# Kernel tuning notes

Hardware: AMD Instinct MI355X
Metric: run time of the kernel (lower is better)

The kernel has to match this reference:

```python
import jax, jax.numpy as jnp
import numpy as np

LN_EPS = 1e-5


def _make_valid_boxes(key, shape):
    # boxes in [x_min, y_min, x_max, y_max] with min < max
    k1, k2 = jax.random.split(key)
    mins = jax.random.uniform(k1, shape, dtype=jnp.float32)            # [.., 2]
    sizes = jax.random.uniform(k2, shape, dtype=jnp.float32) * 0.2 + 1e-3
    return jnp.concatenate([mins, mins + sizes], axis=-1)


def setup_inputs() -> dict:
    key = jax.random.key(0)
    k_t, k_b, k_w = jax.random.split(key, 3)
    N, H = 100000, 768
    target = _make_valid_boxes(k_t, (2,))          # [4]
    ocr_boxes = _make_valid_boxes(k_b, (N, 2))     # [N, 4]
    W = jax.random.normal(k_w, (11, H), dtype=jnp.float32) * (1.0 / np.sqrt(11))
    b = jnp.zeros((H,), dtype=jnp.float32)
    ln_gamma = jnp.ones((H,), dtype=jnp.float32)
    ln_beta = jnp.zeros((H,), dtype=jnp.float32)
    return {"target": target, "ocr_boxes": ocr_boxes, "W": W, "b": b,
            "ln_gamma": ln_gamma, "ln_beta": ln_beta}


def _geo_features(target, boxes):
    # target: [4], boxes: [N, 4]  (x_min, y_min, x_max, y_max)
    tx0, ty0, tx1, ty1 = target[0], target[1], target[2], target[3]
    x0, y0, x1, y1 = boxes[:, 0], boxes[:, 1], boxes[:, 2], boxes[:, 3]
    N = boxes.shape[0]
    ones = jnp.ones((N,), boxes.dtype)

    # HeightWidthRelation: [w1, h1, w2, h2, |w1-w2|, |h1-h2|]
    w1, h1 = tx1 - tx0, ty1 - ty0
    w2, h2 = x1 - x0, y1 - y0
    hw = jnp.stack([w1 * ones, h1 * ones, w2, h2,
                    jnp.abs(w1 - w2), jnp.abs(h1 - h2)], axis=-1)   # [N, 6]

    # Centers
    c1x, c1y = (tx0 + tx1) * 0.5, (ty0 + ty1) * 0.5
    c2x, c2y = (x0 + x1) * 0.5, (y0 + y1) * 0.5
    dx, dy = c2x - c1x, c2y - c1y

    # DistanceRelation: L2 center distance
    dist = jnp.sqrt(dx * dx + dy * dy)                               # [N]

    # IoURelation
    overlap = (tx0 < x1) & (tx1 > x0) & (ty0 < y1) & (ty1 > y0)
    xi0, yi0 = jnp.maximum(tx0, x0), jnp.maximum(ty0, y0)
    xi1, yi1 = jnp.minimum(tx1, x1), jnp.minimum(ty1, y1)
    inter = jnp.where(overlap, (xi1 - xi0) * (yi1 - yi0), 0.0)       # [N]
    a1 = w1 * h1
    a2 = w2 * h2
    union = a1 + a2 - inter
    iou = jnp.stack([inter / union, inter / a1, inter / a2], axis=-1)  # [N, 3]

    # AngleRelation: atan2(|dy|, |dx|) degree bucket (degree in [0, 90])
    degree = jnp.arctan2(jnp.abs(dy), jnp.abs(dx)) * (180.0 / jnp.pi)
    bucket = jnp.where((degree > 22.5) & (degree <= 67.5), 1.0,
             jnp.where((degree > 67.5) & (degree <= 112.5), 2.0,
             jnp.where((degree > 112.5) & (degree <= 157.5), 3.0,
             jnp.where((degree > 157.5) & (degree <= 202.5), 4.0,
             jnp.where((degree > 202.5) & (degree <= 247.5), 5.0,
             jnp.where((degree > 247.5) & (degree <= 292.5), 6.0,
             jnp.where((degree > 292.5) & (degree <= 337.5), 7.0, 8.0)))))))

    return jnp.concatenate([hw, dist[:, None], iou, bucket[:, None]], axis=-1)  # [N, 11]


def reference(target, ocr_boxes, W, b, ln_gamma, ln_beta):
    feats = _geo_features(target, ocr_boxes)            # [N, 11]
    x = feats @ W + b                                   # [N, H]
    mean = jnp.mean(x, axis=-1, keepdims=True)
    var = jnp.mean(jnp.square(x - mean), axis=-1, keepdims=True)
    x = (x - mean) * jax.lax.rsqrt(var + LN_EPS) * ln_gamma + ln_beta
    return jax.nn.relu(x)
```

## Files before the change

### kernel.cpp

```cpp
#include <hip/hip_runtime.h>
#include <math.h>

#define H 768
#define LN_EPS 1e-5f

typedef float nfloat4 __attribute__((ext_vector_type(4)));

__global__ __launch_bounds__(256, 2) void geo_ln_kernel(
    const float* __restrict__ target,
    const float* __restrict__ boxes,
    const float* __restrict__ W,
    const float* __restrict__ bias,
    const float* __restrict__ gamma,
    const float* __restrict__ beta,
    float* __restrict__ out,
    int N)
{
    const int lane = threadIdx.x & 63;
    const int wid  = (blockIdx.x << 2) | (threadIdx.x >> 6);
    const int nw   = gridDim.x << 2;

    const float tx0 = target[0], ty0 = target[1], tx1 = target[2], ty1 = target[3];
    const float w1 = tx1 - tx0, h1 = ty1 - ty0;
    const float c1x = (tx0 + tx1) * 0.5f, c1y = (ty0 + ty1) * 0.5f;
    const float a1 = w1 * h1;
    const float ra1 = 1.0f / a1;
    const float tanA = 0.41421356237309503f;
    const float tanB = 2.41421356237309503f;

    const float4* __restrict__ W4  = reinterpret_cast<const float4*>(W);
    const float4* __restrict__ b4  = reinterpret_cast<const float4*>(bias);
    const float4* __restrict__ g4  = reinterpret_cast<const float4*>(gamma);
    const float4* __restrict__ be4 = reinterpret_cast<const float4*>(beta);
    const float4* __restrict__ boxes4 = reinterpret_cast<const float4*>(boxes);
    nfloat4* __restrict__ outv = reinterpret_cast<nfloat4*>(out);

    float4 base[3], Wr[3][9], gm[3], bt[3];
    #pragma unroll
    for (int r = 0; r < 3; ++r) {
        const int c4 = lane + 64 * r;
        float4 acc = b4[c4];
        const float4 w0 = W4[0 * (H / 4) + c4];
        const float4 w1r = W4[1 * (H / 4) + c4];
        acc.x = fmaf(w1, w0.x, acc.x); acc.y = fmaf(w1, w0.y, acc.y);
        acc.z = fmaf(w1, w0.z, acc.z); acc.w = fmaf(w1, w0.w, acc.w);
        acc.x = fmaf(h1, w1r.x, acc.x); acc.y = fmaf(h1, w1r.y, acc.y);
        acc.z = fmaf(h1, w1r.z, acc.z); acc.w = fmaf(h1, w1r.w, acc.w);
        base[r] = acc;
        #pragma unroll
        for (int k = 0; k < 9; ++k)
            Wr[r][k] = W4[(k + 2) * (H / 4) + c4];
        gm[r] = g4[c4];
        bt[r] = be4[c4];
    }

    auto process = [&](int box) {
        const float4 bx = boxes4[box];
        const float x0 = bx.x, y0 = bx.y, x1 = bx.z, y1 = bx.w;

        float v[9];
        const float w2 = x1 - x0, h2 = y1 - y0;
        v[0] = w2; v[1] = h2;
        v[2] = fabsf(w1 - w2); v[3] = fabsf(h1 - h2);
        const float c2x = (x0 + x1) * 0.5f, c2y = (y0 + y1) * 0.5f;
        const float dx = c2x - c1x, dy = c2y - c1y;
        v[4] = __builtin_amdgcn_sqrtf(dx * dx + dy * dy);
        const bool overlap = (tx0 < x1) && (tx1 > x0) && (ty0 < y1) && (ty1 > y0);
        const float xi0 = fmaxf(tx0, x0), yi0 = fmaxf(ty0, y0);
        const float xi1 = fminf(tx1, x1), yi1 = fminf(ty1, y1);
        const float inter = overlap ? (xi1 - xi0) * (yi1 - yi0) : 0.0f;
        const float a2 = w2 * h2;
        const float uni = a1 + a2 - inter;
        v[5] = inter * __builtin_amdgcn_rcpf(uni);
        v[6] = inter * ra1;
        v[7] = inter * __builtin_amdgcn_rcpf(a2);
        const float adx = fabsf(dx), ady = fabsf(dy);
        v[8] = (ady > adx * tanA) ? ((ady > adx * tanB) ? 2.0f : 1.0f) : 8.0f;

        float4 xv[3];
        float s = 0.0f, sq = 0.0f;
        #pragma unroll
        for (int r = 0; r < 3; ++r) {
            float4 acc = base[r];
            #pragma unroll
            for (int k = 0; k < 9; ++k) {
                const float4 w = Wr[r][k];
                acc.x = fmaf(v[k], w.x, acc.x);
                acc.y = fmaf(v[k], w.y, acc.y);
                acc.z = fmaf(v[k], w.z, acc.z);
                acc.w = fmaf(v[k], w.w, acc.w);
            }
            xv[r] = acc;
            s  += acc.x + acc.y + acc.z + acc.w;
            sq += acc.x * acc.x + acc.y * acc.y + acc.z * acc.z + acc.w * acc.w;
        }

        #pragma unroll
        for (int off = 32; off >= 1; off >>= 1) {
            s  += __shfl_xor(s,  off, 64);
            sq += __shfl_xor(sq, off, 64);
        }
        const float mean = s * (1.0f / H);
        const float var  = sq * (1.0f / H) - mean * mean;
        const float rstd = __builtin_amdgcn_rsqf(var + LN_EPS);

        nfloat4* __restrict__ orow = outv + (size_t)box * (H / 4);
        #pragma unroll
        for (int r = 0; r < 3; ++r) {
            const float4 vx = xv[r];
            const float4 g = gm[r], be = bt[r];
            nfloat4 o;
            o.x = fmaxf(0.0f, (vx.x - mean) * rstd * g.x + be.x);
            o.y = fmaxf(0.0f, (vx.y - mean) * rstd * g.y + be.y);
            o.z = fmaxf(0.0f, (vx.z - mean) * rstd * g.z + be.z);
            o.w = fmaxf(0.0f, (vx.w - mean) * rstd * g.w + be.w);
            __builtin_nontemporal_store(o, &orow[lane + 64 * r]);
        }
    };

    int box = wid;
    for (; box + nw < N; box += 2 * nw) {
        process(box);
        process(box + nw);
    }
    if (box < N) process(box);
}

extern "C" void kernel_launch(void* const* d_in, const int* in_sizes, int n_in,
                              void* d_out, int out_size, void* d_ws, size_t ws_size,
                              hipStream_t stream) {
    const float* target = (const float*)d_in[0];
    const float* boxes  = (const float*)d_in[1];
    const float* W      = (const float*)d_in[2];
    const float* bias   = (const float*)d_in[3];
    const float* gamma  = (const float*)d_in[4];
    const float* beta   = (const float*)d_in[5];
    float* out = (float*)d_out;

    const int N = in_sizes[1] / 4;
    const int grid = 512;

    geo_ln_kernel<<<grid, 256, 0, stream>>>(target, boxes, W, bias, gamma, beta, out, N);
}
```

Baseline: 350.4 us.

## Compute LayerNorm stats analytically via Gram matrix of W and bias

Precomputes the Gram matrix of the weight rows and bias, plus their column means, in a small kernel. A second kernel derives each row's mean and variance in closed form from the 11 features, so the main kernel no longer needs the 64-lane shuffle reductions. The main kernel also prefetches the next boxes and stats one iteration ahead. This adds two extra launches and a stats round-trip through workspace memory, and the E[x^2]-mean^2 form may lose precision.

Measured after the change: 324.5 us. 7.4% less time.

```diff
diff --git a/kernel.cpp b/kernel.cpp
--- a/kernel.cpp
+++ b/kernel.cpp
@@ -6,7 +6,230 @@
 
 typedef float nfloat4 __attribute__((ext_vector_type(4)));
 
+__device__ __forceinline__ void geo_feats(
+    const float4 bx,
+    const float tx0, const float ty0, const float tx1, const float ty1,
+    const float w1, const float h1, const float c1x, const float c1y,
+    const float a1, const float ra1,
+    float* __restrict__ v)
+{
+    const float tanA = 0.41421356237309503f;
+    const float tanB = 2.41421356237309503f;
+    const float x0 = bx.x, y0 = bx.y, x1 = bx.z, y1 = bx.w;
+    const float w2 = x1 - x0, h2 = y1 - y0;
+    v[0] = w2; v[1] = h2;
+    v[2] = fabsf(w1 - w2); v[3] = fabsf(h1 - h2);
+    const float c2x = (x0 + x1) * 0.5f, c2y = (y0 + y1) * 0.5f;
+    const float dx = c2x - c1x, dy = c2y - c1y;
+    v[4] = __builtin_amdgcn_sqrtf(dx * dx + dy * dy);
+    const bool overlap = (tx0 < x1) && (tx1 > x0) && (ty0 < y1) && (ty1 > y0);
+    const float xi0 = fmaxf(tx0, x0), yi0 = fmaxf(ty0, y0);
+    const float xi1 = fminf(tx1, x1), yi1 = fminf(ty1, y1);
+    const float inter = overlap ? (xi1 - xi0) * (yi1 - yi0) : 0.0f;
+    const float a2 = w2 * h2;
+    const float uni = a1 + a2 - inter;
+    v[5] = inter * __builtin_amdgcn_rcpf(uni);
+    v[6] = inter * ra1;
+    v[7] = inter * __builtin_amdgcn_rcpf(a2);
+    const float adx = fabsf(dx), ady = fabsf(dy);
+    v[8] = (ady > adx * tanA) ? ((ady > adx * tanB) ? 2.0f : 1.0f) : 8.0f;
+}
+
+__global__ __launch_bounds__(256) void gram_kernel(
+    const float* __restrict__ W,
+    const float* __restrict__ bias,
+    float* __restrict__ ws)
+{
+    const int i = blockIdx.x;
+    const int tid = threadIdx.x;
+
+    int p = 0, q = 0;
+    const float* A;
+    const float* B = nullptr;
+    if (i < 78) {
+        while ((p + 1) * (p + 2) / 2 <= i) ++p;
+        q = i - p * (p + 1) / 2;
+        A = (p < 11) ? (W + p * H) : bias;
+        B = (q < 11) ? (W + q * H) : bias;
+    } else {
+        p = i - 78;
+        A = (p < 11) ? (W + p * H) : bias;
+    }
+
+    float acc = 0.0f;
+    if (B) {
+        for (int c = tid; c < H; c += 256) acc += A[c] * B[c];
+    } else {
+        for (int c = tid; c < H; c += 256) acc += A[c];
+    }
+
+    #pragma unroll
+    for (int off = 32; off >= 1; off >>= 1) acc += __shfl_xor(acc, off, 64);
+
+    __shared__ float red[4];
+    if ((tid & 63) == 0) red[tid >> 6] = acc;
+    __syncthreads();
+    if (tid == 0) {
+        const float s = ((red[0] + red[1]) + (red[2] + red[3])) * (1.0f / H);
+        if (i < 78) { ws[p * 12 + q] = s; ws[q * 12 + p] = s; }
+        else        { ws[144 + p] = s; }
+    }
+}
+
+__global__ __launch_bounds__(256) void stats_kernel(
+    const float* __restrict__ target,
+    const float* __restrict__ boxes,
+    const float* __restrict__ ws,
+    float2* __restrict__ stats,
+    int N)
+{
+    const float tx0 = target[0], ty0 = target[1], tx1 = target[2], ty1 = target[3];
+    const float w1 = tx1 - tx0, h1 = ty1 - ty0;
+    const float c1x = (tx0 + tx1) * 0.5f, c1y = (ty0 + ty1) * 0.5f;
+    const float a1 = w1 * h1;
+    const float ra1 = 1.0f / a1;
+
+    float Q[9][9], qlin[9], mlin[9];
+    #pragma unroll
+    for (int l = 0; l < 9; ++l)
+        #pragma unroll
+        for (int k = 0; k < 9; ++k)
+            Q[l][k] = ws[(l + 2) * 12 + (k + 2)];
+    #pragma unroll
+    for (int k = 0; k < 9; ++k) {
+        qlin[k] = 2.0f * (w1 * ws[0 * 12 + (k + 2)]
+                        + h1 * ws[1 * 12 + (k + 2)]
+                        +      ws[11 * 12 + (k + 2)]);
+        mlin[k] = ws[144 + k + 2];
+    }
+    const float K = w1 * w1 * ws[0] + 2.0f * w1 * h1 * ws[1] + h1 * h1 * ws[13]
+                  + 2.0f * w1 * ws[11] + 2.0f * h1 * ws[1 * 12 + 11] + ws[11 * 12 + 11];
+    const float mconst = w1 * ws[144] + h1 * ws[145] + ws[155];
+
+    const float4* __restrict__ boxes4 = reinterpret_cast<const float4*>(boxes);
+    const int stride = gridDim.x * blockDim.x;
+    for (int b = blockIdx.x * blockDim.x + threadIdx.x; b < N; b += stride) {
+        const float4 bx = boxes4[b];
+        float v[9];
+        geo_feats(bx, tx0, ty0, tx1, ty1, w1, h1, c1x, c1y, a1, ra1, v);
+
+        float mean = mconst;
+        #pragma unroll
+        for (int k = 0; k < 9; ++k) mean = fmaf(mlin[k], v[k], mean);
+
+        float E = K;
+        #pragma unroll
+        for (int l = 0; l < 9; ++l) {
+            float t = qlin[l];
+            #pragma unroll
+            for (int k = 0; k < 9; ++k) t = fmaf(Q[l][k], v[k], t);
+            E = fmaf(t, v[l], E);
+        }
+
+        const float var  = fmaf(-mean, mean, E);
+        const float rstd = __builtin_amdgcn_rsqf(fmaxf(var, 0.0f) + LN_EPS);
+        float2 st; st.x = rstd; st.y = mean * rstd;
+        stats[b] = st;
+    }
+}
+
 __global__ __launch_bounds__(256, 2) void geo_ln_kernel(
+    const float* __restrict__ target,
+    const float* __restrict__ boxes,
+    const float* __restrict__ W,
+    const float* __restrict__ bias,
+    const float* __restrict__ gamma,
+    const float* __restrict__ beta,
+    const float2* __restrict__ stats,
+    float* __restrict__ out,
+    int N)
+{
+    const int lane = threadIdx.x & 63;
+    const int wid  = (blockIdx.x << 2) | (threadIdx.x >> 6);
+    const int nw   = gridDim.x << 2;
+
+    const float tx0 = target[0], ty0 = target[1], tx1 = target[2], ty1 = target[3];
+    const float w1 = tx1 - tx0, h1 = ty1 - ty0;
+    const float c1x = (tx0 + tx1) * 0.5f, c1y = (ty0 + ty1) * 0.5f;
+    const float a1 = w1 * h1;
+    const float ra1 = 1.0f / a1;
+
+    const float4* __restrict__ W4  = reinterpret_cast<const float4*>(W);
+    const float4* __restrict__ b4  = reinterpret_cast<const float4*>(bias);
+    const float4* __restrict__ g4  = reinterpret_cast<const float4*>(gamma);
+    const float4* __restrict__ be4 = reinterpret_cast<const float4*>(beta);
+    const float4* __restrict__ boxes4 = reinterpret_cast<const float4*>(boxes);
+    nfloat4* __restrict__ outv = reinterpret_cast<nfloat4*>(out);
+
+    float4 base[3], Wr[3][9], gm[3], bt[3];
+    #pragma unroll
+    for (int r = 0; r < 3; ++r) {
+        const int c4 = lane + 64 * r;
+        float4 acc = b4[c4];
+        const float4 w0  = W4[0 * (H / 4) + c4];
+        const float4 w1r = W4[1 * (H / 4) + c4];
+        acc.x = fmaf(w1, w0.x, acc.x); acc.y = fmaf(w1, w0.y, acc.y);
+        acc.z = fmaf(w1, w0.z, acc.z); acc.w = fmaf(w1, w0.w, acc.w);
+        acc.x = fmaf(h1, w1r.x, acc.x); acc.y = fmaf(h1, w1r.y, acc.y);
+        acc.z = fmaf(h1, w1r.z, acc.z); acc.w = fmaf(h1, w1r.w, acc.w);
+        base[r] = acc;
+        #pragma unroll
+        for (int k = 0; k < 9; ++k)
+            Wr[r][k] = W4[(k + 2) * (H / 4) + c4];
+        gm[r] = g4[c4];
+        bt[r] = be4[c4];
+    }
+
+    auto process = [&](const float4 bx, const float2 st, const int box) {
+        float v[9];
+        geo_feats(bx, tx0, ty0, tx1, ty1, w1, h1, c1x, c1y, a1, ra1, v);
+        const float rstd = st.x;
+        const float nmr  = -st.y;
+        nfloat4* __restrict__ orow = outv + (size_t)box * (H / 4);
+        #pragma unroll
+        for (int r = 0; r < 3; ++r) {
+            float4 acc = base[r];
+            #pragma unroll
+            for (int k = 0; k < 9; ++k) {
+                const float4 w = Wr[r][k];
+                acc.x = fmaf(v[k], w.x, acc.x);
+                acc.y = fmaf(v[k], w.y, acc.y);
+                acc.z = fmaf(v[k], w.z, acc.z);
+                acc.w = fmaf(v[k], w.w, acc.w);
+            }
+            const float4 g = gm[r], be = bt[r];
+            nfloat4 o;
+            o.x = fmaxf(0.0f, fmaf(fmaf(acc.x, rstd, nmr), g.x, be.x));
+            o.y = fmaxf(0.0f, fmaf(fmaf(acc.y, rstd, nmr), g.y, be.y));
+            o.z = fmaxf(0.0f, fmaf(fmaf(acc.z, rstd, nmr), g.z, be.z));
+            o.w = fmaxf(0.0f, fmaf(fmaf(acc.w, rstd, nmr), g.w, be.w));
+            __builtin_nontemporal_store(o, &orow[lane + 64 * r]);
+        }
+    };
+
+    int box = wid;
+    if (box >= N) return;
+    float4 bA = boxes4[box];
+    float2 sA = stats[box];
+    bool hasB = (box + nw < N);
+    float4 bB = bA; float2 sB = sA;
+    if (hasB) { bB = boxes4[box + nw]; sB = stats[box + nw]; }
+
+    while (hasB) {
+        const int nxt = box + 2 * nw;
+        const bool hA = (nxt < N), hB = (nxt + nw < N);
+        float4 nA = bA, nB = bB; float2 nsA = sA, nsB = sB;
+        if (hA) { nA = boxes4[nxt];      nsA = stats[nxt]; }
+        if (hB) { nB = boxes4[nxt + nw]; nsB = stats[nxt + nw]; }
+        process(bA, sA, box);
+        process(bB, sB, box + nw);
+        bA = nA; sA = nsA; bB = nB; sB = nsB;
+        box = nxt; hasB = hB;
+    }
+    if (box < N) process(bA, sA, box);
+}
+
+__global__ __launch_bounds__(256, 2) void geo_ln_fallback(
     const float* __restrict__ target,
     const float* __restrict__ boxes,
     const float* __restrict__ W,
@@ -25,8 +248,6 @@
     const float c1x = (tx0 + tx1) * 0.5f, c1y = (ty0 + ty1) * 0.5f;
     const float a1 = w1 * h1;
     const float ra1 = 1.0f / a1;
-    const float tanA = 0.41421356237309503f;
-    const float tanB = 2.41421356237309503f;
 
     const float4* __restrict__ W4  = reinterpret_cast<const float4*>(W);
     const float4* __restrict__ b4  = reinterpret_cast<const float4*>(bias);
@@ -40,7 +261,7 @@
     for (int r = 0; r < 3; ++r) {
         const int c4 = lane + 64 * r;
         float4 acc = b4[c4];
-        const float4 w0 = W4[0 * (H / 4) + c4];
+        const float4 w0  = W4[0 * (H / 4) + c4];
         const float4 w1r = W4[1 * (H / 4) + c4];
         acc.x = fmaf(w1, w0.x, acc.x); acc.y = fmaf(w1, w0.y, acc.y);
         acc.z = fmaf(w1, w0.z, acc.z); acc.w = fmaf(w1, w0.w, acc.w);
@@ -56,26 +277,8 @@
 
     auto process = [&](int box) {
         const float4 bx = boxes4[box];
-        const float x0 = bx.x, y0 = bx.y, x1 = bx.z, y1 = bx.w;
-
         float v[9];
-        const float w2 = x1 - x0, h2 = y1 - y0;
-        v[0] = w2; v[1] = h2;
-        v[2] = fabsf(w1 - w2); v[3] = fabsf(h1 - h2);
-        const float c2x = (x0 + x1) * 0.5f, c2y = (y0 + y1) * 0.5f;
-        const float dx = c2x - c1x, dy = c2y - c1y;
-        v[4] = __builtin_amdgcn_sqrtf(dx * dx + dy * dy);
-        const bool overlap = (tx0 < x1) && (tx1 > x0) && (ty0 < y1) && (ty1 > y0);
-        const float xi0 = fmaxf(tx0, x0), yi0 = fmaxf(ty0, y0);
-        const float xi1 = fminf(tx1, x1), yi1 = fminf(ty1, y1);
-        const float inter = overlap ? (xi1 - xi0) * (yi1 - yi0) : 0.0f;
-        const float a2 = w2 * h2;
-        const float uni = a1 + a2 - inter;
-        v[5] = inter * __builtin_amdgcn_rcpf(uni);
-        v[6] = inter * ra1;
-        v[7] = inter * __builtin_amdgcn_rcpf(a2);
-        const float adx = fabsf(dx), ady = fabsf(dy);
-        v[8] = (ady > adx * tanA) ? ((ady > adx * tanB) ? 2.0f : 1.0f) : 8.0f;
+        geo_feats(bx, tx0, ty0, tx1, ty1, w1, h1, c1x, c1y, a1, ra1, v);
 
         float4 xv[3];
         float s = 0.0f, sq = 0.0f;
@@ -138,7 +341,23 @@
     float* out = (float*)d_out;
 
     const int N = in_sizes[1] / 4;
-    const int grid = 512;
-
-    geo_ln_kernel<<<grid, 256, 0, stream>>>(target, boxes, W, bias, gamma, beta, out, N);
-}
+
+    const size_t needed = (160 + 2 * (size_t)N) * sizeof(float);
+
+    if (d_ws && ws_size >= needed && N > 0) {
+        float* wsf = (float*)d_ws;
+        float2* stats = (float2*)(wsf + 160);
+
+        gram_kernel<<<90, 256, 0, stream>>>(W, bias, wsf);
+
+        int blocksA2 = (N + 255) / 256;
+        if (blocksA2 > 2048) blocksA2 = 2048;
+        stats_kernel<<<blocksA2, 256, 0, stream>>>(target, boxes, wsf, stats, N);
+
+        geo_ln_kernel<<<512, 256, 0, stream>>>(target, boxes, W, bias, gamma, beta,
+                                               stats, out, N);
+    } else {
+        geo_ln_fallback<<<512, 256, 0, stream>>>(target, boxes, W, bias, gamma, beta,
+                                                 out, N);
+    }
+}
```
